# Performance work log

Measured on AMD Instinct MI355X. Metric: run time of the kernel, lower is better.

## Reference

```python
import jax, jax.numpy as jnp
import numpy as np

B, T, D, H = 8, 1024, 512, 8
D4 = 4 * D
SIGMA = 16.0
EPS = 1e-5


def layer_norm(x, w, b):
    m = jnp.mean(x, axis=-1, keepdims=True)
    v = jnp.mean((x - m) ** 2, axis=-1, keepdims=True)
    return (x - m) * jax.lax.rsqrt(v + EPS) * w + b


def setup_inputs() -> dict:
    key = jax.random.key(0)
    ks = jax.random.split(key, 12)
    return {
        "x": jax.random.normal(ks[0], (B, T, D), jnp.float32),
        "posv": jax.random.randint(ks[1], (B, T), 0, 64, jnp.int32),
        "posh": jax.random.randint(ks[2], (B, T), 0, 64, jnp.int32),
        "norm1_w": jnp.ones((D,), jnp.float32),
        "norm1_b": jnp.zeros((D,), jnp.float32),
        "in_w": jax.random.normal(ks[3], (3 * D, D), jnp.float32) * (D ** -0.5),
        "in_b": jnp.zeros((3 * D,), jnp.float32),
        "out_w": jax.random.normal(ks[4], (D, D), jnp.float32) * (D ** -0.5),
        "out_b": jnp.zeros((D,), jnp.float32),
        "norm2_w": jnp.ones((D,), jnp.float32),
        "norm2_b": jnp.zeros((D,), jnp.float32),
        "w1": jax.random.normal(ks[5], (D4, D), jnp.float32) * (D ** -0.5),
        "b1": jnp.zeros((D4,), jnp.float32),
        "w2": jax.random.normal(ks[6], (D, D4), jnp.float32) * (D4 ** -0.5),
        "b2": jnp.zeros((D,), jnp.float32),
        "gate": jnp.array(0.0, jnp.float32),
    }


def reference(x, posv, posh, norm1_w, norm1_b, in_w, in_b, out_w, out_b,
              norm2_w, norm2_b, w1, b1, w2, b2, gate):
    hd = D // H
    residual = x
    xn = layer_norm(x, norm1_w, norm1_b)

    # --- standard multi-head self-attention (dropout=eval identity) ---
    qkv = xn @ in_w.T + in_b                       # [B,T,3D]
    q, k, v = jnp.split(qkv, 3, axis=-1)
    q = q.reshape(B, T, H, hd).transpose(0, 2, 1, 3)  # [B,H,T,hd]
    k = k.reshape(B, T, H, hd).transpose(0, 2, 1, 3)
    v = v.reshape(B, T, H, hd).transpose(0, 2, 1, 3)
    scores = jnp.einsum("bhqd,bhkd->bhqk", q, k) * (hd ** -0.5)
    attn = jax.nn.softmax(scores, axis=-1)
    ctx = jnp.einsum("bhqk,bhkd->bhqd", attn, v)   # [B,H,T,hd]
    ctx = ctx.transpose(0, 2, 1, 3).reshape(B, T, D)
    std_out = ctx @ out_w.T + out_b

    # --- Gaussian kernel position attention ---
    pos = jnp.stack([posv, posh], axis=-1).astype(jnp.float32)  # [B,T,2]
    dist_sq = jnp.sum((pos[:, :, None, :] - pos[:, None, :, :]) ** 2, axis=-1)  # [B,T,T]
    kw = jnp.exp(-dist_sq / (2.0 * SIGMA ** 2))
    kw = kw / jnp.sum(kw, axis=-1, keepdims=True)
    kernel_out = kw @ xn                            # [B,T,D]

    g = jax.nn.sigmoid(gate)
    x1 = residual + g * std_out + (1.0 - g) * kernel_out

    # --- MLP block ---
    xn2 = layer_norm(x1, norm2_w, norm2_b)
    h = jax.nn.gelu(xn2 @ w1.T + b1, approximate=False)
    return x1 + h @ w2.T + b2
```

## Files before the change

### kernel.cpp

```cpp
#include <hip/hip_runtime.h>
#include <hip/hip_bf16.h>
#include <math.h>

typedef unsigned short ushort_t;
typedef short short8 __attribute__((ext_vector_type(8)));
typedef float f32x4 __attribute__((ext_vector_type(4)));

__device__ __forceinline__ float b2f(ushort_t u) {
  union { unsigned u; float f; } v; v.u = ((unsigned)u) << 16; return v.f;
}
__device__ __forceinline__ ushort_t f2b(float f) {
  union { float f; unsigned u; } v; v.f = f;
  unsigned r = (v.u + 0x7FFFu + ((v.u >> 16) & 1u)) >> 16;
  return (ushort_t)r;
}
__device__ __forceinline__ float gelu_fast(float v) {
  float u = 0.7978845608f * (v + 0.044715f * v * v * v);
  float a = fabsf(u);
  float t = exp2f(a * -2.8853900817779268f);
  float th = (1.f - t) / (1.f + t);
  th = copysignf(th, u);
  return 0.5f * v * (1.f + th);
}

union U16x8 { uint4 v; ushort_t s[8]; };

typedef const __attribute__((address_space(1))) unsigned int glb_u32;
typedef __attribute__((address_space(3))) unsigned int lds_u32;
__device__ __forceinline__ void gl_lds16(const ushort_t* g, ushort_t* l) {
  __builtin_amdgcn_global_load_lds((glb_u32*)g, (lds_u32*)l, 16, 0, 0);
}

__global__ __launch_bounds__(256) void prep_kernel(const float* __restrict__ s0,
                                                   const float* __restrict__ s1,
                                                   const float* __restrict__ s2,
                                                   const float* __restrict__ s3,
                                                   ushort_t* __restrict__ d0,
                                                   ushort_t* __restrict__ d1,
                                                   ushort_t* __restrict__ d2,
                                                   ushort_t* __restrict__ d3,
                                                   const float* __restrict__ x,
                                                   const float* __restrict__ w,
                                                   const float* __restrict__ b,
                                                   ushort_t* __restrict__ xnout,
                                                   const int* __restrict__ posv,
                                                   const int* __restrict__ posh,
                                                   ushort_t* __restrict__ kw) {
  int bid = blockIdx.x;
  int tid = threadIdx.x;
  if (bid < 3072) {
    long i = (long)bid * 256 + tid;
    const float* s; ushort_t* d; long off;
    if (i < 196608)       { s = s0; d = d0; off = i; }
    else if (i < 262144)  { s = s1; d = d1; off = i - 196608; }
    else if (i < 524288)  { s = s2; d = d2; off = i - 262144; }
    else                  { s = s3; d = d3; off = i - 524288; }
    float4 f = *(const float4*)(s + off * 4);
    union { uint2 v; ushort_t s[4]; } o;
    o.s[0] = f2b(f.x); o.s[1] = f2b(f.y); o.s[2] = f2b(f.z); o.s[3] = f2b(f.w);
    *(uint2*)(d + off * 4) = o.v;
  } else if (bid < 5120) {
    int wave = tid >> 6, lane = tid & 63;
    long token = (long)(bid - 3072) * 4 + wave;
    const float* xr = x + token * 512 + lane * 8;
    float4 a0 = *(const float4*)xr;
    float4 a1 = *(const float4*)(xr + 4);
    float xf[8] = {a0.x, a0.y, a0.z, a0.w, a1.x, a1.y, a1.z, a1.w};
    float s = 0.f, sq = 0.f;
#pragma unroll
    for (int i = 0; i < 8; i++) { s += xf[i]; sq += xf[i] * xf[i]; }
#pragma unroll
    for (int off = 1; off < 64; off <<= 1) { s += __shfl_xor(s, off); sq += __shfl_xor(sq, off); }
    float m = s * (1.f / 512.f);
    float var = sq * (1.f / 512.f) - m * m;
    float rs = rsqrtf(var + 1e-5f);
    float4 w0 = *(const float4*)(w + lane * 8);
    float4 w1v = *(const float4*)(w + lane * 8 + 4);
    float4 b0 = *(const float4*)(b + lane * 8);
    float4 b1v = *(const float4*)(b + lane * 8 + 4);
    float wf[8] = {w0.x, w0.y, w0.z, w0.w, w1v.x, w1v.y, w1v.z, w1v.w};
    float bf[8] = {b0.x, b0.y, b0.z, b0.w, b1v.x, b1v.y, b1v.z, b1v.w};
    U16x8 o;
#pragma unroll
    for (int i = 0; i < 8; i++) o.s[i] = f2b((xf[i] - m) * rs * wf[i] + bf[i]);
    *(uint4*)(xnout + token * 512 + lane * 8) = o.v;
  } else {
    int bb = bid - 5120;
    int bz = bb >> 10, i = bb & 1023;
    const int* pv = posv + bz * 1024;
    const int* ph = posh + bz * 1024;
    int pvi = pv[i], phi = ph[i];
    int j0 = tid * 4;
    int4 vj = *(const int4*)(pv + j0);
    int4 hj = *(const int4*)(ph + j0);
    int vv[4] = {vj.x, vj.y, vj.z, vj.w};
    int hh[4] = {hj.x, hj.y, hj.z, hj.w};
    float e[4]; float loc = 0.f;
#pragma unroll
    for (int u = 0; u < 4; u++) {
      int dv = pvi - vv[u], dh = phi - hh[u];
      e[u] = expf((float)(dv * dv + dh * dh) * (-1.f / 512.f));
      loc += e[u];
    }
#pragma unroll
    for (int off = 1; off < 64; off <<= 1) loc += __shfl_xor(loc, off);
    __shared__ float wsum[4];
    __shared__ float tot;
    if ((tid & 63) == 0) wsum[tid >> 6] = loc;
    __syncthreads();
    if (tid == 0) tot = wsum[0] + wsum[1] + wsum[2] + wsum[3];
    __syncthreads();
    float inv = 1.f / tot;
    union { uint2 v; ushort_t s[4]; } o;
#pragma unroll
    for (int u = 0; u < 4; u++) o.s[u] = f2b(e[u] * inv);
    *(uint2*)&kw[((long)(bz * 1024 + i)) * 1024 + j0] = o.v;
  }
}

__global__ __launch_bounds__(256) void ln_b_kernel(const ushort_t* __restrict__ x,
                                                   const float* __restrict__ w,
                                                   const float* __restrict__ b,
                                                   ushort_t* __restrict__ out) {
  int tid = threadIdx.x, wave = tid >> 6, lane = tid & 63;
  long token = (long)blockIdx.x * 4 + wave;
  U16x8 ux; ux.v = *(const uint4*)(x + token * 512 + lane * 8);
  float xf[8], s = 0.f, sq = 0.f;
#pragma unroll
  for (int i = 0; i < 8; i++) { xf[i] = b2f(ux.s[i]); s += xf[i]; sq += xf[i] * xf[i]; }
#pragma unroll
  for (int off = 1; off < 64; off <<= 1) { s += __shfl_xor(s, off); sq += __shfl_xor(sq, off); }
  float m = s * (1.f / 512.f);
  float var = sq * (1.f / 512.f) - m * m;
  float rs = rsqrtf(var + 1e-5f);
  float4 w0 = *(const float4*)(w + lane * 8);
  float4 w1v = *(const float4*)(w + lane * 8 + 4);
  float4 b0 = *(const float4*)(b + lane * 8);
  float4 b1v = *(const float4*)(b + lane * 8 + 4);
  float wf[8] = {w0.x, w0.y, w0.z, w0.w, w1v.x, w1v.y, w1v.z, w1v.w};
  float bf[8] = {b0.x, b0.y, b0.z, b0.w, b1v.x, b1v.y, b1v.z, b1v.w};
  U16x8 o;
#pragma unroll
  for (int i = 0; i < 8; i++) o.s[i] = f2b((xf[i] - m) * rs * wf[i] + bf[i]);
  *(uint4*)(out + token * 512 + lane * 8) = o.v;
}

__global__ __launch_bounds__(256) void tr2_kernel(const ushort_t* __restrict__ in0,
                                                  ushort_t* __restrict__ out0,
                                                  const ushort_t* __restrict__ in1,
                                                  ushort_t* __restrict__ out1) {
  __shared__ ushort_t tile[64 * 64];
  int b = blockIdx.x;
  const ushort_t* src; ushort_t* dst; int C, r0, c0;
  if (b < 1024) {
    int z = b >> 4; r0 = (b & 15) * 64; c0 = 0; C = 64;
    src = in0 + (long)z * 1024 * 64; dst = out0 + (long)z * 1024 * 64;
  } else {
    int bb = b - 1024;
    int z = bb >> 7; r0 = ((bb >> 3) & 15) * 64; c0 = (bb & 7) * 64; C = 512;
    src = in1 + (long)z * 1024 * 512; dst = out1 + (long)z * 1024 * 512;
  }
  int R = 1024;
  int tid = threadIdx.x;
  int tr = tid >> 2;
  const ushort_t* s = src + (long)(r0 + tr) * C + c0;
  int g = (tr + (tr >> 4)) & 7;
#pragma unroll
  for (int u = 0; u < 2; u++) {
    int c = (tid & 3) + u * 4;
    *(uint4*)&tile[tr * 64 + (c ^ g) * 8] = *(const uint4*)(s + c * 8);
  }
  __syncthreads();
  int oc = tid >> 2, ob = (tid & 3) * 16;
  U16x8 o0, o1;
#pragma unroll
  for (int j = 0; j < 16; j++) {
    int r = ob + j;
    int gg = (r + (r >> 4)) & 7;
    ushort_t val = tile[r * 64 + (((oc >> 3) ^ gg)) * 8 + (oc & 7)];
    if (j < 8) o0.s[j] = val; else o1.s[j - 8] = val;
  }
  ushort_t* d = dst + (long)(c0 + oc) * R + r0 + ob;
  *(uint4*)d = o0.v;
  *(uint4*)(d + 8) = o1.v;
}

struct GemmP {
  const ushort_t* A; const ushort_t* Bm;
  long sA, sB, sC;
  int lda, ldb, ldc, K;
  const float* biasf;
  const float* residf;
  const ushort_t* auxb;
  float* outf;
  ushort_t* outb;
  ushort_t* qp; ushort_t* kp; ushort_t* vp;
  const float* gate;
};

template <int BM, int BN, int EPI>
__global__ __launch_bounds__(256) void gemm_k(GemmP p) {
  constexpr int TI = BM / 32, TJ = BN / 32;
  constexpr int RA = BM / 64, RB = BN / 64;
  __shared__ ushort_t As[4][BM * 32];
  __shared__ ushort_t Bs[4][BN * 32];
  int tid = threadIdx.x, wv = tid >> 6, lane = tid & 63;
  int quad = lane >> 4, l15 = lane & 15;
  int bl = blockIdx.x + gridDim.x * blockIdx.y;
  int m0 = (bl % gridDim.y) * BM;
  int n0 = (bl / gridDim.y) * BN;
  int z = blockIdx.z;
  const ushort_t* A = p.A + (long)z * p.sA;
  const ushort_t* Bm = p.Bm + (long)z * p.sB;
  int wm = (wv & 1) * (BM / 2), wn = (wv >> 1) * (BN / 2);
  f32x4 acc[TI][TJ];
#pragma unroll
  for (int i = 0; i < TI; i++)
#pragma unroll
    for (int j = 0; j < TJ; j++)
#pragma unroll
      for (int r = 0; r < 4; r++) acc[i][j][r] = 0.f;

  int srow = tid >> 2;
  int sc = ((tid & 3) ^ ((tid >> 3) & 3)) * 8;
  const ushort_t* ga = A + (long)(m0 + srow) * p.lda + sc;
  const ushort_t* gb = Bm + (long)(n0 + srow) * p.ldb + sc;
  long a64 = (long)64 * p.lda, b64 = (long)64 * p.ldb;
  int aswz = (quad ^ ((l15 >> 1) & 3)) * 8;
  int nsteps = p.K >> 5;

#pragma unroll
  for (int s = 0; s < 2; s++) {
#pragma unroll
    for (int rr = 0; rr < RA; rr++)
      gl_lds16(ga + s * 32 + rr * a64, As[s] + rr * 2048 + wv * 512);
#pragma unroll
    for (int rr = 0; rr < RB; rr++)
      gl_lds16(gb + s * 32 + rr * b64, Bs[s] + rr * 2048 + wv * 512);
  }

  for (int ks = 0; ks < nsteps; ks += 2) {
    asm volatile("s_waitcnt vmcnt(0)" ::: "memory");
    __builtin_amdgcn_s_barrier();
    if (ks + 2 < nsteps) {
#pragma unroll
      for (int s = 0; s < 2; s++) {
        int st = ks + 2 + s, bf = st & 3;
        const ushort_t* a0 = ga + st * 32;
        const ushort_t* b0 = gb + st * 32;
#pragma unroll
        for (int rr = 0; rr < RA; rr++)
          gl_lds16(a0 + rr * a64, As[bf] + rr * 2048 + wv * 512);
#pragma unroll
        for (int rr = 0; rr < RB; rr++)
          gl_lds16(b0 + rr * b64, Bs[bf] + rr * 2048 + wv * 512);
      }
    }
#pragma unroll
    for (int hs = 0; hs < 2; hs++) {
      int cur = (ks + hs) & 3;
      short8 av[TI], bv[TJ];
#pragma unroll
      for (int ti = 0; ti < TI; ti++)
        av[ti] = *(const short8*)&As[cur][(wm + ti * 16 + l15) * 32 + aswz];
#pragma unroll
      for (int tj = 0; tj < TJ; tj++)
        bv[tj] = *(const short8*)&Bs[cur][(wn + tj * 16 + l15) * 32 + aswz];
#pragma unroll
      for (int ti = 0; ti < TI; ti++)
#pragma unroll
        for (int tj = 0; tj < TJ; tj++)
          acc[ti][tj] = __builtin_amdgcn_mfma_f32_16x16x32_bf16(av[ti], bv[tj], acc[ti][tj], 0, 0, 0);
    }
  }

  float g = 0.f;
  if constexpr (EPI == 2) g = 1.f / (1.f + expf(-p.gate[0]));
#pragma unroll
  for (int ti = 0; ti < TI; ti++) {
#pragma unroll
    for (int tj = 0; tj < TJ; tj++) {
#pragma unroll
      for (int r = 0; r < 4; r++) {
        int gm = m0 + wm + ti * 16 + quad * 4 + r;
        int n = n0 + wn + tj * 16 + l15;
        float v = acc[ti][tj][r];
        if constexpr (EPI == 0) {
          v += p.biasf[n];
          int bb = gm >> 10, tt = gm & 1023;
          if (n < 512) {
            int h = n >> 6, d = n & 63;
            p.qp[((long)(bb * 8 + h) * 1024 + tt) * 64 + d] = f2b(v * 0.18033688011112042f);
          } else if (n < 1024) {
            int n2 = n - 512, h = n2 >> 6, d = n2 & 63;
            p.kp[((long)(bb * 8 + h) * 1024 + tt) * 64 + d] = f2b(v);
          } else {
            int n2 = n - 1024, h = n2 >> 6, d = n2 & 63;
            p.vp[((long)(bb * 8 + h) * 1024 + tt) * 64 + d] = f2b(v);
          }
        } else if constexpr (EPI == 2) {
          v += p.biasf[n];
          long idx = (long)gm * 512 + n;
          p.outb[idx] = f2b(p.residf[idx] + g * v + (1.f - g) * b2f(p.auxb[idx]));
        } else if constexpr (EPI == 3) {
          v += p.biasf[n];
          p.outb[(long)gm * p.ldc + n] = f2b(gelu_fast(v));
        } else {
          v += p.biasf[n];
          long idx = (long)gm * 512 + n;
          p.outf[idx] = v + b2f(p.auxb[idx]);
        }
      }
    }
  }
}

__global__ __launch_bounds__(256) void fk_kernel(const ushort_t* __restrict__ q,
                                                 const ushort_t* __restrict__ k,
                                                 const ushort_t* __restrict__ vT,
                                                 ushort_t* __restrict__ ctx,
                                                 const ushort_t* __restrict__ kwp,
                                                 const ushort_t* __restrict__ xnT,
                                                 ushort_t* __restrict__ ko) {
  __shared__ __align__(16) ushort_t smem[24576];
  int b = blockIdx.x;
  int tid = threadIdx.x, wv = tid >> 6, lane = tid & 63;
  int quad = lane >> 4, l15 = lane & 15;

  if (b < 512) {
    int bh = b & 63;
    int q0 = (b >> 6) * 128;
    ushort_t* Ksp = smem;
    ushort_t* Vtp = smem + 8192;
    ushort_t* Ptp = smem + 16384;
    int wm = wv * 32;

    short8 qf[2][2];
#pragma unroll
    for (int tq = 0; tq < 2; tq++)
#pragma unroll
      for (int kk2 = 0; kk2 < 2; kk2++)
        qf[tq][kk2] = *(const short8*)&q[((long)bh * 1024 + q0 + wm + tq * 16 + l15) * 64 + kk2 * 32 + quad * 8];

    int srow = tid >> 3;
    int sc = ((tid & 7) ^ ((tid >> 3) & 7)) * 8;
#pragma unroll
    for (int e = 0; e < 2; e++) {
      gl_lds16(&k[((long)bh * 1024 + e * 32 + srow) * 64 + sc], Ksp + e * 2048 + wv * 512);
      gl_lds16(&vT[((long)bh * 64 + e * 32 + srow) * 1024 + sc], Vtp + e * 2048 + wv * 512);
    }

    f32x4 O[2][4];
#pragma unroll
    for (int tq = 0; tq < 2; tq++)
#pragma unroll
      for (int td = 0; td < 4; td++)
#pragma unroll
        for (int r = 0; r < 4; r++) O[tq][td][r] = 0.f;
    float ls[2] = {0.f, 0.f};

    int pswz = (l15 & 7) << 1;
    for (int kt = 0; kt < 16; kt++) {
      int cur = kt & 1;
      asm volatile("s_waitcnt vmcnt(0)" ::: "memory");
      __builtin_amdgcn_s_barrier();
      if (kt + 1 < 16) {
#pragma unroll
        for (int e = 0; e < 2; e++) {
          gl_lds16(&k[((long)bh * 1024 + (kt + 1) * 64 + e * 32 + srow) * 64 + sc], Ksp + (cur ^ 1) * 4096 + e * 2048 + wv * 512);
          gl_lds16(&vT[((long)bh * 64 + e * 32 + srow) * 1024 + (kt + 1) * 64 + sc], Vtp + (cur ^ 1) * 4096 + e * 2048 + wv * 512);
        }
      }
#pragma unroll
      for (int tq = 0; tq < 2; tq++) {
        f32x4 S[4];
#pragma unroll
        for (int tk = 0; tk < 4; tk++) {
#pragma unroll
          for (int r = 0; r < 4; r++) S[tk][r] = 0.f;
#pragma unroll
          for (int kk2 = 0; kk2 < 2; kk2++) {
            short8 kf = *(const short8*)&Ksp[cur * 4096 + (tk * 16 + l15) * 64 + ((kk2 * 4 + quad) ^ (l15 & 7)) * 8];
            S[tk] = __builtin_amdgcn_mfma_f32_16x16x32_bf16(kf, qf[tq][kk2], S[tk], 0, 0, 0);
          }
        }
#pragma unroll
        for (int tk = 0; tk < 4; tk++) {
          float p0 = exp2f(S[tk][0]);
          float p1 = exp2f(S[tk][1]);
          float p2 = exp2f(S[tk][2]);
          float p3 = exp2f(S[tk][3]);
          ls[tq] += (p0 + p1) + (p2 + p3);
          unsigned lo = __builtin_amdgcn_perm(__float_as_uint(p1), __float_as_uint(p0), 0x07060302u);
          unsigned hi = __builtin_amdgcn_perm(__float_as_uint(p3), __float_as_uint(p2), 0x07060302u);
          int gnum = (tk * 4 + quad) ^ pswz;
          uint2 pr; pr.x = lo; pr.y = hi;
          *(uint2*)&Ptp[(wm + tq * 16 + l15) * 64 + gnum * 4] = pr;
        }
      }
#pragma unroll
      for (int tq = 0; tq < 2; tq++) {
#pragma unroll
        for (int kk2 = 0; kk2 < 2; kk2++) {
          short8 pf = *(const short8*)&Ptp[(wm + tq * 16 + l15) * 64 + (((kk2 * 8 + quad * 2) ^ pswz)) * 4];
#pragma unroll
          for (int td = 0; td < 4; td++) {
            short8 vf = *(const short8*)&Vtp[cur * 4096 + (td * 16 + l15) * 64 + ((kk2 * 4 + quad) ^ (l15 & 7)) * 8];
            O[tq][td] = __builtin_amdgcn_mfma_f32_16x16x32_bf16(pf, vf, O[tq][td], 0, 0, 0);
          }
        }
      }
    }
#pragma unroll
    for (int tq = 0; tq < 2; tq++) {
      ls[tq] += __shfl_xor(ls[tq], 16);
      ls[tq] += __shfl_xor(ls[tq], 32);
    }
    int bb = bh >> 3, h = bh & 7;
#pragma unroll
    for (int tq = 0; tq < 2; tq++) {
#pragma unroll
      for (int r = 0; r < 4; r++) {
        int qrow = quad * 4 + r;
        float inv = 1.f / __shfl(ls[tq], (lane & 48) | qrow);
        long row = (long)bb * 1024 + q0 + wm + tq * 16 + qrow;
#pragma unroll
        for (int td = 0; td < 4; td++)
          ctx[row * 512 + h * 64 + td * 16 + l15] = f2b(O[tq][td][r] * inv);
      }
    }
  } else {
    int b2 = b - 512;
    int z = b2 >> 6, bl = b2 & 63;
    int m0 = (bl & 15) * 64;
    int n0 = (bl >> 4) * 128;
    const ushort_t* A = kwp + (long)z * (1024L * 1024);
    const ushort_t* Bm = xnT + (long)z * (512L * 1024);
    ushort_t* Asp = smem;
    ushort_t* Bsp = smem + 8192;
    int wm = (wv & 1) * 32, wn = (wv >> 1) * 64;
    f32x4 acc[2][4];
#pragma unroll
    for (int i = 0; i < 2; i++)
#pragma unroll
      for (int j = 0; j < 4; j++)
#pragma unroll
        for (int r = 0; r < 4; r++) acc[i][j][r] = 0.f;

    int srow = tid >> 2;
    int sc = ((tid & 3) ^ ((tid >> 3) & 3)) * 8;
    const ushort_t* ga = A + (long)(m0 + srow) * 1024 + sc;
    const ushort_t* gb = Bm + (long)(n0 + srow) * 1024 + sc;
    const long a64 = 64L * 1024, b64 = 64L * 1024;
    int aswz = (quad ^ ((l15 >> 1) & 3)) * 8;

#pragma unroll
    for (int s = 0; s < 2; s++) {
      gl_lds16(ga + s * 32, Asp + s * 2048 + wv * 512);
#pragma unroll
      for (int rr = 0; rr < 2; rr++)
        gl_lds16(gb + s * 32 + rr * b64, Bsp + s * 4096 + rr * 2048 + wv * 512);
    }

    for (int ks = 0; ks < 32; ks += 2) {
      asm volatile("s_waitcnt vmcnt(0)" ::: "memory");
      __builtin_amdgcn_s_barrier();
      if (ks + 2 < 32) {
#pragma unroll
        for (int s = 0; s < 2; s++) {
          int st = ks + 2 + s, bf = st & 3;
          gl_lds16(ga + st * 32, Asp + bf * 2048 + wv * 512);
#pragma unroll
          for (int rr = 0; rr < 2; rr++)
            gl_lds16(gb + st * 32 + rr * b64, Bsp + bf * 4096 + rr * 2048 + wv * 512);
        }
      }
#pragma unroll
      for (int hs = 0; hs < 2; hs++) {
        int cur = (ks + hs) & 3;
        short8 av[2], bv[4];
#pragma unroll
        for (int ti = 0; ti < 2; ti++)
          av[ti] = *(const short8*)&Asp[cur * 2048 + (wm + ti * 16 + l15) * 32 + aswz];
#pragma unroll
        for (int tj = 0; tj < 4; tj++)
          bv[tj] = *(const short8*)&Bsp[cur * 4096 + (wn + tj * 16 + l15) * 32 + aswz];
#pragma unroll
        for (int ti = 0; ti < 2; ti++)
#pragma unroll
          for (int tj = 0; tj < 4; tj++)
            acc[ti][tj] = __builtin_amdgcn_mfma_f32_16x16x32_bf16(av[ti], bv[tj], acc[ti][tj], 0, 0, 0);
      }
    }

#pragma unroll
    for (int ti = 0; ti < 2; ti++) {
#pragma unroll
      for (int tj = 0; tj < 4; tj++) {
#pragma unroll
        for (int r = 0; r < 4; r++) {
          int gm = m0 + wm + ti * 16 + quad * 4 + r;
          int n = n0 + wn + tj * 16 + l15;
          ko[(long)z * (1024L * 512) + (long)gm * 512 + n] = f2b(acc[ti][tj][r]);
        }
      }
    }
  }
}

extern "C" void kernel_launch(void* const* d_in, const int* in_sizes, int n_in,
                              void* d_out, int out_size, void* d_ws, size_t ws_size,
                              hipStream_t stream) {
  const float* x    = (const float*)d_in[0];
  const int* posv   = (const int*)d_in[1];
  const int* posh   = (const int*)d_in[2];
  const float* n1w  = (const float*)d_in[3];
  const float* n1b  = (const float*)d_in[4];
  const float* in_w = (const float*)d_in[5];
  const float* in_b = (const float*)d_in[6];
  const float* outw = (const float*)d_in[7];
  const float* outb = (const float*)d_in[8];
  const float* n2w  = (const float*)d_in[9];
  const float* n2b  = (const float*)d_in[10];
  const float* w1   = (const float*)d_in[11];
  const float* b1   = (const float*)d_in[12];
  const float* w2   = (const float*)d_in[13];
  const float* b2   = (const float*)d_in[14];
  const float* gate = (const float*)d_in[15];
  float* out = (float*)d_out;

  char* ws = (char*)d_ws;
  const size_t MB = 1024 * 1024;
  ushort_t* q    = (ushort_t*)(ws + 0 * MB);
  ushort_t* kk   = (ushort_t*)(ws + 8 * MB);
  ushort_t* vtmp = (ushort_t*)(ws + 16 * MB);
  ushort_t* vT   = (ushort_t*)(ws + 24 * MB);
  ushort_t* kw   = (ushort_t*)(ws + 32 * MB);
  ushort_t* xn   = (ushort_t*)(ws + 48 * MB);
  ushort_t* xnT  = (ushort_t*)(ws + 56 * MB);
  ushort_t* ctx  = (ushort_t*)(ws + 64 * MB);
  ushort_t* ko   = (ushort_t*)(ws + 72 * MB);
  ushort_t* x1b  = (ushort_t*)(ws + 80 * MB);
  ushort_t* xn2  = (ushort_t*)(ws + 16 * MB);
  ushort_t* inwb = (ushort_t*)(ws + 96 * MB);
  ushort_t* owb  = (ushort_t*)(ws + 98 * MB);
  ushort_t* w1b  = (ushort_t*)(ws + 99 * MB);
  ushort_t* w2b  = (ushort_t*)(ws + 101 * MB);
  ushort_t* h    = (ushort_t*)(ws + 24 * MB);

  prep_kernel<<<13312, 256, 0, stream>>>(in_w, outw, w1, w2, inwb, owb, w1b, w2b,
                                         x, n1w, n1b, xn, posv, posh, kw);
  {
    GemmP p = {};
    p.A = xn; p.Bm = inwb; p.lda = 512; p.ldb = 512; p.K = 512;
    p.biasf = in_b; p.qp = q; p.kp = kk; p.vp = vtmp;
    gemm_k<64, 128, 0><<<dim3(12, 128, 1), 256, 0, stream>>>(p);
  }
  tr2_kernel<<<2048, 256, 0, stream>>>(vtmp, vT, xn, xnT);
  fk_kernel<<<1024, 256, 0, stream>>>(q, kk, vT, ctx, kw, xnT, ko);
  {
    GemmP p = {};
    p.A = ctx; p.Bm = owb; p.lda = 512; p.ldb = 512; p.K = 512;
    p.biasf = outb; p.residf = x; p.auxb = ko; p.outb = x1b; p.gate = gate;
    gemm_k<64, 64, 2><<<dim3(8, 128, 1), 256, 0, stream>>>(p);
  }
  ln_b_kernel<<<2048, 256, 0, stream>>>(x1b, n2w, n2b, xn2);
  {
    GemmP p = {};
    p.A = xn2; p.Bm = w1b; p.lda = 512; p.ldb = 512; p.ldc = 2048; p.K = 512;
    p.biasf = b1; p.outb = h;
    gemm_k<64, 128, 3><<<dim3(16, 128, 1), 256, 0, stream>>>(p);
  }
  {
    GemmP p = {};
    p.A = h; p.Bm = w2b; p.lda = 2048; p.ldb = 2048; p.K = 2048;
    p.biasf = b2; p.auxb = x1b; p.outf = out;
    gemm_k<64, 128, 4><<<dim3(4, 128, 1), 256, 0, stream>>>(p);
  }
}
```

Baseline: 266.6 us.

## Fuse QKV GEMM with xn transpose and write V transposed directly

The QKV projection GEMM and the transpose kernel are merged into one launch. The first 1536 blocks do the GEMM and write V straight into its transposed [B,H,d,T] layout, which removes the intermediate V buffer and its separate transpose pass. The remaining 1024 blocks transpose xn. This saves a kernel launch and a round trip of V through memory. The cost is that the transposed V stores are strided along T, so they coalesce poorly, and the larger shared-memory footprint applies to the transpose blocks too.

After: 267.2 us. Within noise of the previous version (+0.2%).

```diff
diff --git a/kernel.cpp b/kernel.cpp
--- a/kernel.cpp
+++ b/kernel.cpp
@@ -145,44 +145,129 @@
   *(uint4*)(out + token * 512 + lane * 8) = o.v;
 }
 
-__global__ __launch_bounds__(256) void tr2_kernel(const ushort_t* __restrict__ in0,
-                                                  ushort_t* __restrict__ out0,
-                                                  const ushort_t* __restrict__ in1,
-                                                  ushort_t* __restrict__ out1) {
-  __shared__ ushort_t tile[64 * 64];
-  int b = blockIdx.x;
-  const ushort_t* src; ushort_t* dst; int C, r0, c0;
-  if (b < 1024) {
-    int z = b >> 4; r0 = (b & 15) * 64; c0 = 0; C = 64;
-    src = in0 + (long)z * 1024 * 64; dst = out0 + (long)z * 1024 * 64;
+__global__ __launch_bounds__(256) void qt_kernel(const ushort_t* __restrict__ xn,
+                                                 const ushort_t* __restrict__ inwb,
+                                                 const float* __restrict__ in_b,
+                                                 ushort_t* __restrict__ qp,
+                                                 ushort_t* __restrict__ kp,
+                                                 ushort_t* __restrict__ vTp,
+                                                 ushort_t* __restrict__ xnT) {
+  __shared__ __align__(16) ushort_t smem[24576];
+  int bid = blockIdx.x;
+  int tid = threadIdx.x, wv = tid >> 6, lane = tid & 63;
+  int quad = lane >> 4, l15 = lane & 15;
+
+  if (bid < 1536) {
+    ushort_t* As = smem;
+    ushort_t* Bs = smem + 8192;
+    int m0 = (bid & 127) * 64;
+    int n0 = (bid >> 7) * 128;
+    int wm = (wv & 1) * 32, wn = (wv >> 1) * 64;
+    f32x4 acc[2][4];
+#pragma unroll
+    for (int i = 0; i < 2; i++)
+#pragma unroll
+      for (int j = 0; j < 4; j++)
+#pragma unroll
+        for (int r = 0; r < 4; r++) acc[i][j][r] = 0.f;
+
+    int srow = tid >> 2;
+    int sc = ((tid & 3) ^ ((tid >> 3) & 3)) * 8;
+    const ushort_t* ga = xn + (long)(m0 + srow) * 512 + sc;
+    const ushort_t* gb = inwb + (long)(n0 + srow) * 512 + sc;
+    const long a64 = 64L * 512, b64 = 64L * 512;
+    int aswz = (quad ^ ((l15 >> 1) & 3)) * 8;
+
+#pragma unroll
+    for (int s = 0; s < 2; s++) {
+      gl_lds16(ga + s * 32, As + s * 2048 + wv * 512);
+#pragma unroll
+      for (int rr = 0; rr < 2; rr++)
+        gl_lds16(gb + s * 32 + rr * b64, Bs + s * 4096 + rr * 2048 + wv * 512);
+    }
+
+    for (int ks = 0; ks < 16; ks += 2) {
+      asm volatile("s_waitcnt vmcnt(0)" ::: "memory");
+      __builtin_amdgcn_s_barrier();
+      if (ks + 2 < 16) {
+#pragma unroll
+        for (int s = 0; s < 2; s++) {
+          int st = ks + 2 + s, bf = st & 3;
+          gl_lds16(ga + st * 32, As + bf * 2048 + wv * 512);
+#pragma unroll
+          for (int rr = 0; rr < 2; rr++)
+            gl_lds16(gb + st * 32 + rr * b64, Bs + bf * 4096 + rr * 2048 + wv * 512);
+        }
+      }
+#pragma unroll
+      for (int hs = 0; hs < 2; hs++) {
+        int cur = (ks + hs) & 3;
+        short8 av[2], bv[4];
+#pragma unroll
+        for (int ti = 0; ti < 2; ti++)
+          av[ti] = *(const short8*)&As[cur * 2048 + (wm + ti * 16 + l15) * 32 + aswz];
+#pragma unroll
+        for (int tj = 0; tj < 4; tj++)
+          bv[tj] = *(const short8*)&Bs[cur * 4096 + (wn + tj * 16 + l15) * 32 + aswz];
+#pragma unroll
+        for (int ti = 0; ti < 2; ti++)
+#pragma unroll
+          for (int tj = 0; tj < 4; tj++)
+            acc[ti][tj] = __builtin_amdgcn_mfma_f32_16x16x32_bf16(av[ti], bv[tj], acc[ti][tj], 0, 0, 0);
+      }
+    }
+
+#pragma unroll
+    for (int ti = 0; ti < 2; ti++) {
+#pragma unroll
+      for (int tj = 0; tj < 4; tj++) {
+#pragma unroll
+        for (int r = 0; r < 4; r++) {
+          int gm = m0 + wm + ti * 16 + quad * 4 + r;
+          int n = n0 + wn + tj * 16 + l15;
+          float v = acc[ti][tj][r] + in_b[n];
+          int bb = gm >> 10, tt = gm & 1023;
+          if (n < 512) {
+            int h = n >> 6, d = n & 63;
+            qp[((long)(bb * 8 + h) * 1024 + tt) * 64 + d] = f2b(v * 0.18033688011112042f);
+          } else if (n < 1024) {
+            int n2 = n - 512, h = n2 >> 6, d = n2 & 63;
+            kp[((long)(bb * 8 + h) * 1024 + tt) * 64 + d] = f2b(v);
+          } else {
+            int n2 = n - 1024, h = n2 >> 6, d = n2 & 63;
+            vTp[((long)(bb * 8 + h) * 64 + d) * 1024 + tt] = f2b(v);
+          }
+        }
+      }
+    }
   } else {
-    int bb = b - 1024;
-    int z = bb >> 7; r0 = ((bb >> 3) & 15) * 64; c0 = (bb & 7) * 64; C = 512;
-    src = in1 + (long)z * 1024 * 512; dst = out1 + (long)z * 1024 * 512;
-  }
-  int R = 1024;
-  int tid = threadIdx.x;
-  int tr = tid >> 2;
-  const ushort_t* s = src + (long)(r0 + tr) * C + c0;
-  int g = (tr + (tr >> 4)) & 7;
-#pragma unroll
-  for (int u = 0; u < 2; u++) {
-    int c = (tid & 3) + u * 4;
-    *(uint4*)&tile[tr * 64 + (c ^ g) * 8] = *(const uint4*)(s + c * 8);
-  }
-  __syncthreads();
-  int oc = tid >> 2, ob = (tid & 3) * 16;
-  U16x8 o0, o1;
-#pragma unroll
-  for (int j = 0; j < 16; j++) {
-    int r = ob + j;
-    int gg = (r + (r >> 4)) & 7;
-    ushort_t val = tile[r * 64 + (((oc >> 3) ^ gg)) * 8 + (oc & 7)];
-    if (j < 8) o0.s[j] = val; else o1.s[j - 8] = val;
-  }
-  ushort_t* d = dst + (long)(c0 + oc) * R + r0 + ob;
-  *(uint4*)d = o0.v;
-  *(uint4*)(d + 8) = o1.v;
+    ushort_t* tile = smem;
+    int b2 = bid - 1536;
+    int z = b2 >> 7, r0 = ((b2 >> 3) & 15) * 64, c0 = (b2 & 7) * 64;
+    const ushort_t* src = xn + (long)z * 1024 * 512;
+    ushort_t* dst = xnT + (long)z * 1024 * 512;
+    int tr = tid >> 2;
+    const ushort_t* s = src + (long)(r0 + tr) * 512 + c0;
+    int g = (tr + (tr >> 4)) & 7;
+#pragma unroll
+    for (int u = 0; u < 2; u++) {
+      int c = (tid & 3) + u * 4;
+      *(uint4*)&tile[tr * 64 + (c ^ g) * 8] = *(const uint4*)(s + c * 8);
+    }
+    __syncthreads();
+    int oc = tid >> 2, ob = (tid & 3) * 16;
+    U16x8 o0, o1;
+#pragma unroll
+    for (int j = 0; j < 16; j++) {
+      int r = ob + j;
+      int gg = (r + (r >> 4)) & 7;
+      ushort_t val = tile[r * 64 + (((oc >> 3) ^ gg)) * 8 + (oc & 7)];
+      if (j < 8) o0.s[j] = val; else o1.s[j - 8] = val;
+    }
+    ushort_t* d = dst + (long)(c0 + oc) * 1024 + r0 + ob;
+    *(uint4*)d = o0.v;
+    *(uint4*)(d + 8) = o1.v;
+  }
 }
 
 struct GemmP {
@@ -209,9 +294,8 @@
   int bl = blockIdx.x + gridDim.x * blockIdx.y;
   int m0 = (bl % gridDim.y) * BM;
   int n0 = (bl / gridDim.y) * BN;
-  int z = blockIdx.z;
-  const ushort_t* A = p.A + (long)z * p.sA;
-  const ushort_t* Bm = p.Bm + (long)z * p.sB;
+  const ushort_t* A = p.A;
+  const ushort_t* Bm = p.Bm;
   int wm = (wv & 1) * (BM / 2), wn = (wv >> 1) * (BN / 2);
   f32x4 acc[TI][TJ];
 #pragma unroll
@@ -285,20 +369,7 @@
         int gm = m0 + wm + ti * 16 + quad * 4 + r;
         int n = n0 + wn + tj * 16 + l15;
         float v = acc[ti][tj][r];
-        if constexpr (EPI == 0) {
-          v += p.biasf[n];
-          int bb = gm >> 10, tt = gm & 1023;
-          if (n < 512) {
-            int h = n >> 6, d = n & 63;
-            p.qp[((long)(bb * 8 + h) * 1024 + tt) * 64 + d] = f2b(v * 0.18033688011112042f);
-          } else if (n < 1024) {
-            int n2 = n - 512, h = n2 >> 6, d = n2 & 63;
-            p.kp[((long)(bb * 8 + h) * 1024 + tt) * 64 + d] = f2b(v);
-          } else {
-            int n2 = n - 1024, h = n2 >> 6, d = n2 & 63;
-            p.vp[((long)(bb * 8 + h) * 1024 + tt) * 64 + d] = f2b(v);
-          }
-        } else if constexpr (EPI == 2) {
+        if constexpr (EPI == 2) {
           v += p.biasf[n];
           long idx = (long)gm * 512 + n;
           p.outb[idx] = f2b(p.residf[idx] + g * v + (1.f - g) * b2f(p.auxb[idx]));
@@ -533,7 +604,6 @@
   const size_t MB = 1024 * 1024;
   ushort_t* q    = (ushort_t*)(ws + 0 * MB);
   ushort_t* kk   = (ushort_t*)(ws + 8 * MB);
-  ushort_t* vtmp = (ushort_t*)(ws + 16 * MB);
   ushort_t* vT   = (ushort_t*)(ws + 24 * MB);
   ushort_t* kw   = (ushort_t*)(ws + 32 * MB);
   ushort_t* xn   = (ushort_t*)(ws + 48 * MB);
@@ -550,13 +620,7 @@
 
   prep_kernel<<<13312, 256, 0, stream>>>(in_w, outw, w1, w2, inwb, owb, w1b, w2b,
                                          x, n1w, n1b, xn, posv, posh, kw);
-  {
-    GemmP p = {};
-    p.A = xn; p.Bm = inwb; p.lda = 512; p.ldb = 512; p.K = 512;
-    p.biasf = in_b; p.qp = q; p.kp = kk; p.vp = vtmp;
-    gemm_k<64, 128, 0><<<dim3(12, 128, 1), 256, 0, stream>>>(p);
-  }
-  tr2_kernel<<<2048, 256, 0, stream>>>(vtmp, vT, xn, xnT);
+  qt_kernel<<<2560, 256, 0, stream>>>(xn, inwb, in_b, q, kk, vT, xnT);
   fk_kernel<<<1024, 256, 0, stream>>>(q, kk, vT, ctx, kw, xnT, ko);
   {
     GemmP p = {};
```
